# Kernel tuning notes

Measured on AMD Instinct MI355X. Metric: run time of the kernel, lower is better.

Reference implementation:

```python
import jax, jax.numpy as jnp
import numpy as np

L, D, DC, T, FF = 512, 512, 256, 128, 2048
P_COEF = 0.5


def layernorm(x, g, b):
    m = jnp.mean(x, axis=-1, keepdims=True)
    v = jnp.mean((x - m) ** 2, axis=-1, keepdims=True)
    return (x - m) / jnp.sqrt(v + 1e-5) * g + b


def conv_pool(t, w):
    # t: (L, N, D); torch attention_pool: permute -> (N, L, D), Conv1d over channels=L, length=D
    x = jnp.transpose(t, (1, 0, 2))  # (N, L, D)
    y = jax.lax.conv_general_dilated(x, w, window_strides=(2,), padding=[(1, 1)],
                                     dimension_numbers=("NCH", "OIH", "NCH"))
    return jnp.transpose(y, (1, 0, 2))  # (L, N, D//2)


def attn_fused(q, k):
    # q: (L, 1, d), k: (M, 1, d); faithful to module.attention with N=1 (squeeze(1))
    q2, k2 = q[:, 0], k[:, 0]
    scale = 1.0 / jnp.sqrt(jnp.asarray(q2.shape[1], q2.dtype))
    a = jax.nn.softmax((q2 @ k2.T) * scale, axis=-1)
    return (a @ k2 + q2)[:, None, :]  # fused residual add of q


def setup_inputs() -> dict:
    key = jax.random.key(0)
    ks = jax.random.split(key, 8)
    x = jax.random.normal(ks[0], (L, 1, D), jnp.float32)
    cached_k = jax.random.normal(ks[1], (T, L, 1, DC), jnp.float32)
    mem_mask = jax.random.randint(ks[2], (T,), 0, 2, jnp.int32)
    return {
        "x": x,
        "cached_k": cached_k,
        "ln1_g": jnp.ones((D,), jnp.float32),
        "ln1_b": jnp.zeros((D,), jnp.float32),
        "ln2_g": jnp.ones((D,), jnp.float32),
        "ln2_b": jnp.zeros((D,), jnp.float32),
        "w_compress_k": jax.random.normal(ks[3], (L, L, 3), jnp.float32) * (1.0 / np.sqrt(3 * L)),
        "w_compress_cur": jax.random.normal(ks[4], (L, L, 3), jnp.float32) * (1.0 / np.sqrt(3 * L)),
        "ap_w": jax.random.normal(ks[5], (DC, D), jnp.float32) * (1.0 / np.sqrt(DC)),
        "ap_b": jnp.zeros((D,), jnp.float32),
        "fc_w": jax.random.normal(ks[6], (D, FF), jnp.float32) * (1.0 / np.sqrt(D)),
        "fc_b": jnp.zeros((FF,), jnp.float32),
        "proj_w": jax.random.normal(ks[7], (FF, D), jnp.float32) * (1.0 / np.sqrt(FF)),
        "proj_b": jnp.zeros((D,), jnp.float32),
        "mem_mask": mem_mask,
    }


def reference(x, cached_k, ln1_g, ln1_b, ln2_g, ln2_b, w_compress_k, w_compress_cur,
              ap_w, ap_b, fc_w, fc_b, proj_w, proj_b, mem_mask):
    x1 = layernorm(x, ln1_g, ln1_b)                      # ln_1; q = k = x1
    # mask_memory: zero cached entries whose video name differs (per-entry, N=1)
    mem = cached_k * mem_mask.astype(x.dtype)[:, None, None, None]  # (T, L, 1, DC)
    k_cur = conv_pool(x1, w_compress_cur)                # (L, 1, DC) compress current k
    k = jnp.concatenate([mem.reshape(-1, 1, DC), k_cur], axis=0)    # ((T+1)*L, 1, DC)
    q = conv_pool(x1, w_compress_k)                      # k.shape[2]==256 branch: compress q
    selfatten = attn_fused(q, q)
    atten = attn_fused(q, k) + selfatten * P_COEF
    atten = atten @ ap_w + ap_b                          # attenproj 256 -> 512
    x2 = x1 + atten
    h = layernorm(x2, ln2_g, ln2_b)
    h = h @ fc_w + fc_b
    h = h * jax.nn.sigmoid(1.702 * h)                    # QuickGELU
    h = h @ proj_w + proj_b
    return x2 + h
```

## Files before the change

### kernel.cpp

```cpp
#include <hip/hip_runtime.h>
#include <hip/hip_bf16.h>

typedef unsigned short u16;
typedef unsigned int u32;
typedef __attribute__((ext_vector_type(8))) short bf16x8;
typedef __attribute__((ext_vector_type(4))) short bf16x4;
typedef __attribute__((ext_vector_type(4))) float f32x4;
typedef __attribute__((ext_vector_type(8))) u16 u16x8;
typedef __attribute__((ext_vector_type(4))) u16 u16x4;
typedef __attribute__((ext_vector_type(4))) u32 u32x4;

__device__ __forceinline__ u16 f2bf(float x){
  __hip_bfloat16 h = __float2bfloat16(x);
  return __builtin_bit_cast(u16, h);
}
__device__ __forceinline__ float bf2f(u16 u){
  __hip_bfloat16 h = __builtin_bit_cast(__hip_bfloat16, u);
  return __bfloat162float(h);
}

template<bool BF>
__global__ __launch_bounds__(256) void ln_kernel(const float* __restrict__ in,
    const float* __restrict__ g, const float* __restrict__ b,
    float* __restrict__ outf, u16* __restrict__ outb)
{
  int row = blockIdx.x, tid = threadIdx.x;
  const float* p = in + (size_t)row*512 + tid*2;
  float v0 = p[0], v1 = p[1];
  float s = v0+v1, ss = v0*v0+v1*v1;
  #pragma unroll
  for (int o=1;o<64;o<<=1){ s += __shfl_xor(s,o); ss += __shfl_xor(ss,o); }
  __shared__ float rs[4], rss[4];
  if ((tid&63)==0){ rs[tid>>6]=s; rss[tid>>6]=ss; }
  __syncthreads();
  s = rs[0]+rs[1]+rs[2]+rs[3]; ss = rss[0]+rss[1]+rss[2]+rss[3];
  float mean = s*(1.f/512.f);
  float var  = ss*(1.f/512.f) - mean*mean;
  float rstd = 1.f/sqrtf(var + 1e-5f);
  int d = tid*2;
  float o0 = (v0-mean)*rstd*g[d]   + b[d];
  float o1 = (v1-mean)*rstd*g[d+1] + b[d+1];
  if (BF){
    outb[(size_t)row*512+d]   = f2bf(o0);
    outb[(size_t)row*512+d+1] = f2bf(o1);
  } else {
    outf[(size_t)row*512+d]   = o0;
    outf[(size_t)row*512+d+1] = o1;
  }
}

__global__ __launch_bounds__(256) void xgT_kernel(const float* __restrict__ x1, u16* __restrict__ xgT)
{
  int h = blockIdx.x, tid = threadIdx.x;
  #pragma unroll
  for (int rep=0;rep<6;rep++){
    int k = rep*256 + tid;
    int i = k/3, kk = k - i*3;
    int pos = 2*h - 1 + kk;
    float v = (pos >= 0 && pos < 512) ? x1[(size_t)i*512 + pos] : 0.f;
    xgT[(size_t)h*1536 + k] = f2bf(v);
  }
}

__device__ __forceinline__ void transcvt_body(float (*t)[33],
    const float* __restrict__ in, u16* __restrict__ out, int K, int N, int bx, int by)
{
  int nb = bx*32, kb = by*32;
  int tx = threadIdx.x & 31, ty = threadIdx.x >> 5;
  #pragma unroll
  for (int i=0;i<32;i+=8) t[ty+i][tx] = in[(size_t)(kb+ty+i)*N + nb+tx];
  __syncthreads();
  #pragma unroll
  for (int i=0;i<32;i+=8) out[(size_t)(nb+ty+i)*K + kb+tx] = f2bf(t[tx][ty+i]);
}

__global__ __launch_bounds__(256) void prep_kernel(
    const float* __restrict__ x, const float* __restrict__ ln1g, const float* __restrict__ ln1b,
    const float* __restrict__ wk, const float* __restrict__ wc,
    const float* __restrict__ apw, const float* __restrict__ fcw, const float* __restrict__ pjw,
    const float* __restrict__ ck, const int* __restrict__ mask,
    float* __restrict__ x1,
    u16* __restrict__ wkcb, u16* __restrict__ apT, u16* __restrict__ fcT,
    u16* __restrict__ pjT, u16* __restrict__ kbf)
{
  __shared__ float t[32][33];
  __shared__ float rs[4], rss[4];
  int b = blockIdx.x, tid = threadIdx.x;
  if (b < 512){
    const float* p = x + (size_t)b*512 + tid*2;
    float v0 = p[0], v1 = p[1];
    float s = v0+v1, ss = v0*v0+v1*v1;
    #pragma unroll
    for (int o=1;o<64;o<<=1){ s += __shfl_xor(s,o); ss += __shfl_xor(ss,o); }
    if ((tid&63)==0){ rs[tid>>6]=s; rss[tid>>6]=ss; }
    __syncthreads();
    s = rs[0]+rs[1]+rs[2]+rs[3]; ss = rss[0]+rss[1]+rss[2]+rss[3];
    float mean = s*(1.f/512.f);
    float var  = ss*(1.f/512.f) - mean*mean;
    float rstd = 1.f/sqrtf(var + 1e-5f);
    int d = tid*2;
    x1[(size_t)b*512+d]   = (v0-mean)*rstd*ln1g[d]   + ln1b[d];
    x1[(size_t)b*512+d+1] = (v1-mean)*rstd*ln1g[d+1] + ln1b[d+1];
  } else if (b < 8704){
    int flat = (b-512)*256 + tid;
    int row = flat >> 5, seg = flat & 31;
    if (mask[row>>9] == 0) return;
    const float* src = ck + (size_t)row*256 + seg*8;
    u16x8 o;
    #pragma unroll
    for (int j=0;j<8;j++) o[j] = f2bf(src[j]);
    *(u16x8*)(kbf + (size_t)row*256 + seg*8) = o;
  } else if (b < 9472){
    size_t i = (size_t)((b-8704)*256 + tid)*8;
    const size_t half = (size_t)512*1536;
    const float* src = (i < half) ? (wk + i) : (wc + (i - half));
    u16x8 o;
    #pragma unroll
    for (int j=0;j<8;j++) o[j] = f2bf(src[j]);
    *(u16x8*)(wkcb + i) = o;
  } else if (b < 9600){
    int f = b - 9472;
    transcvt_body(t, apw, apT, 256, 512, f & 15, f >> 4);
  } else if (b < 10624){
    int f = b - 9600;
    transcvt_body(t, fcw, fcT, 512, 2048, f & 63, f >> 6);
  } else {
    int f = b - 10624;
    transcvt_body(t, pjw, pjT, 2048, 512, f & 15, f >> 4);
  }
}

template<int ACT, bool WF32, bool WBF, int W>
__global__ __launch_bounds__(64*W) void gemm4(
    const u16* __restrict__ A, const u16* __restrict__ B,
    const float* __restrict__ bias, const float* __restrict__ resid,
    float* __restrict__ outF, u16* __restrict__ outB, u16* __restrict__ outB2,
    int rowSplit, int M, int N, int K)
{
  __shared__ float red[W][32][33];
  int tid = threadIdx.x;
  int w = tid >> 6, lane = tid & 63;
  int lq = lane & 15, lg = lane >> 4;
  int m0 = blockIdx.y*32, n0 = blockIdx.x*32;
  int Ks = K / W;
  int kbeg = w * Ks;
  f32x4 acc00={0,0,0,0}, acc01={0,0,0,0}, acc10={0,0,0,0}, acc11={0,0,0,0};
  const u16* pa0 = A + (size_t)(m0+lq)*K + kbeg + lg*8;
  const u16* pa1 = pa0 + (size_t)16*K;
  const u16* pb0 = B + (size_t)(n0+lq)*K + kbeg + lg*8;
  const u16* pb1 = pb0 + (size_t)16*K;
  #pragma unroll 2
  for (int k0=0;k0<Ks;k0+=32){
    bf16x8 a0 = *(const bf16x8*)(pa0+k0);
    bf16x8 a1 = *(const bf16x8*)(pa1+k0);
    bf16x8 b0 = *(const bf16x8*)(pb0+k0);
    bf16x8 b1 = *(const bf16x8*)(pb1+k0);
    acc00 = __builtin_amdgcn_mfma_f32_16x16x32_bf16(a0,b0,acc00,0,0,0);
    acc01 = __builtin_amdgcn_mfma_f32_16x16x32_bf16(a0,b1,acc01,0,0,0);
    acc10 = __builtin_amdgcn_mfma_f32_16x16x32_bf16(a1,b0,acc10,0,0,0);
    acc11 = __builtin_amdgcn_mfma_f32_16x16x32_bf16(a1,b1,acc11,0,0,0);
  }
  f32x4 accs[2][2] = {{acc00,acc01},{acc10,acc11}};
  #pragma unroll
  for (int mi=0;mi<2;mi++)
    #pragma unroll
    for (int ni=0;ni<2;ni++)
      #pragma unroll
      for (int r=0;r<4;r++)
        red[w][mi*16+lg*4+r][ni*16+lq] = accs[mi][ni][r];
  __syncthreads();
  #pragma unroll
  for (int rr=0;rr<16/W;rr++){
    int cell = rr*64*W + tid;
    int row = cell >> 5, col = cell & 31;
    float v = 0.f;
    #pragma unroll
    for (int ww=0;ww<W;ww++) v += red[ww][row][col];
    int grow = m0 + row, gcol = n0 + col;
    if (bias)  v += bias[gcol];
    if (ACT==1) v = v/(1.f+__expf(-1.702f*v));
    if (resid) v += resid[(size_t)grow*N+gcol];
    if (WF32) outF[(size_t)grow*N+gcol] = v;
    if (WBF){
      if (grow < rowSplit) outB[(size_t)grow*N+gcol] = f2bf(v);
      else                 outB2[(size_t)(grow-rowSplit)*N+gcol] = f2bf(v);
    }
  }
}

__global__ __launch_bounds__(128) void attn_flash(
    const u16* __restrict__ qb, const u16* __restrict__ keys,
    const int* __restrict__ mask,
    u16* __restrict__ pO, float* __restrict__ pL)
{
  __shared__ u16 kv[2][8192];
  int tid = threadIdx.x;
  int w = tid >> 6, lane = tid & 63, lq = lane & 15, lg = lane >> 4;
  int c = blockIdx.x, qt = blockIdx.y;
  const u16* kp = keys;
  int kstart = c * 1024, off = 0, nt = 32;
  if (c == 65) { kp = qb; kstart = 0; nt = 16; }
  else if (c == 64) { kstart = 65536; nt = 16; }
  else {
    int m0 = mask[2*c], m1 = mask[2*c+1];
    if (!m0 && !m1) return;
    off = m0 ? 0 : 512;
    nt = ((m0 && m1) ? 32 : 16);
  }
  int qbase = qt*32 + w*16;

  bf16x8 qf[8];
  {
    const u16* qrow = qb + (size_t)(qbase+lq)*256 + lg*8;
    #pragma unroll
    for (int s=0;s<8;s++) qf[s] = *(const bf16x8*)(qrow + s*32);
  }
  f32x4 o[16];
  #pragma unroll
  for (int i=0;i<16;i++) o[i] = (f32x4){0,0,0,0};
  float l_acc = 0.f;

  auto kv3 = (__attribute__((address_space(3))) char*)&kv[0][0];
  unsigned kvaddr0 = (unsigned)(unsigned long long)kv3;
  const char* gbase = (const char*)kp + (size_t)(kstart+off)*512;

  #define STAGE(i, b) { \
    const char* tb = gbase + (size_t)(i)*16384; \
    _Pragma("unroll") \
    for (int rep=0; rep<8; rep++){ \
      int slot = rep*128 + tid; \
      int goff = ((slot&63)>>1)*512 + ((slot>>6)*16 + (slot&1)*8)*2; \
      __builtin_amdgcn_global_load_lds( \
        (const __attribute__((address_space(1))) unsigned*)(tb + goff), \
        (__attribute__((address_space(3))) unsigned*)(kv3 + (b)*16384 + (rep*128 + (tid & ~63))*16), \
        16, 0, 0); \
    } }

  #define ISSUE8(T, ab) \
    asm volatile( \
      "ds_read_b64_tr_b16 %0, %8 offset:0\n\t" \
      "ds_read_b64_tr_b16 %1, %8 offset:512\n\t" \
      "ds_read_b64_tr_b16 %2, %8 offset:1024\n\t" \
      "ds_read_b64_tr_b16 %3, %8 offset:1536\n\t" \
      "ds_read_b64_tr_b16 %4, %8 offset:2048\n\t" \
      "ds_read_b64_tr_b16 %5, %8 offset:2560\n\t" \
      "ds_read_b64_tr_b16 %6, %8 offset:3072\n\t" \
      "ds_read_b64_tr_b16 %7, %8 offset:3584\n\t" \
      : "=&v"(T[0]),"=&v"(T[1]),"=&v"(T[2]),"=&v"(T[3]), \
        "=&v"(T[4]),"=&v"(T[5]),"=&v"(T[6]),"=&v"(T[7]) \
      : "v"(ab) : "memory")

  #define MFMA4(T, base) { \
    bf16x8 v0_ = __builtin_shufflevector(T[0],T[1],0,1,2,3,4,5,6,7); \
    bf16x8 v1_ = __builtin_shufflevector(T[2],T[3],0,1,2,3,4,5,6,7); \
    bf16x8 v2_ = __builtin_shufflevector(T[4],T[5],0,1,2,3,4,5,6,7); \
    bf16x8 v3_ = __builtin_shufflevector(T[6],T[7],0,1,2,3,4,5,6,7); \
    o[(base)+0] = __builtin_amdgcn_mfma_f32_16x16x32_bf16(pa, v0_, o[(base)+0], 0,0,0); \
    o[(base)+1] = __builtin_amdgcn_mfma_f32_16x16x32_bf16(pa, v1_, o[(base)+1], 0,0,0); \
    o[(base)+2] = __builtin_amdgcn_mfma_f32_16x16x32_bf16(pa, v2_, o[(base)+2], 0,0,0); \
    o[(base)+3] = __builtin_amdgcn_mfma_f32_16x16x32_bf16(pa, v3_, o[(base)+3], 0,0,0); \
  }

  STAGE(0, 0);
  for (int i=0; i<nt; i++){
    int cur = i & 1;
    if (i+1 < nt){
      STAGE(i+1, cur^1);
      asm volatile("s_waitcnt vmcnt(8)" ::: "memory");
    } else {
      asm volatile("s_waitcnt vmcnt(0)" ::: "memory");
    }
    __syncthreads();

    const u16* kb = &kv[cur][0];
    f32x4 s0 = {0,0,0,0}, s1 = {0,0,0,0};
    #pragma unroll
    for (int s=0;s<8;s++){
      int e = (2*s + (lg>>1))*512 + lq*16 + (lg&1)*8;
      bf16x8 ka0 = *(const bf16x8*)(kb + e);
      bf16x8 ka1 = *(const bf16x8*)(kb + e + 256);
      s0 = __builtin_amdgcn_mfma_f32_16x16x32_bf16(ka0, qf[s], s0, 0,0,0);
      s1 = __builtin_amdgcn_mfma_f32_16x16x32_bf16(ka1, qf[s], s1, 0,0,0);
    }
    asm volatile("s_waitcnt lgkmcnt(0)" ::: "memory");

    unsigned trb = kvaddr0 + cur*16384 + lane*8;
    bf16x4 tA[8], tB[8], tC[8], tD[8];
    ISSUE8(tA, trb);
    ISSUE8(tB, trb + 4096);

    float p[8];
    #pragma unroll
    for (int r=0;r<4;r++){ p[r]   = __expf(s0[r]*0.0625f);
                           p[4+r] = __expf(s1[r]*0.0625f); }
    l_acc += (p[0]+p[1])+(p[2]+p[3])+((p[4]+p[5])+(p[6]+p[7]));
    u32 w0 = (u32)f2bf(p[0]) | ((u32)f2bf(p[1])<<16);
    u32 w1 = (u32)f2bf(p[2]) | ((u32)f2bf(p[3])<<16);
    u32 w2 = (u32)f2bf(p[4]) | ((u32)f2bf(p[5])<<16);
    u32 w3 = (u32)f2bf(p[6]) | ((u32)f2bf(p[7])<<16);
    u32x4 fq = {w0,w1,w2,w3};
    bf16x8 pa = __builtin_bit_cast(bf16x8, fq);

    asm volatile("s_waitcnt lgkmcnt(8)" ::: "memory");
    __builtin_amdgcn_sched_barrier(0);
    MFMA4(tA, 0);
    ISSUE8(tC, trb + 8192);
    asm volatile("s_waitcnt lgkmcnt(8)" ::: "memory");
    __builtin_amdgcn_sched_barrier(0);
    MFMA4(tB, 4);
    ISSUE8(tD, trb + 12288);
    asm volatile("s_waitcnt lgkmcnt(8)" ::: "memory");
    __builtin_amdgcn_sched_barrier(0);
    MFMA4(tC, 8);
    asm volatile("s_waitcnt lgkmcnt(0)" ::: "memory");
    __builtin_amdgcn_sched_barrier(0);
    MFMA4(tD, 12);
    __syncthreads();
  }
  #undef STAGE
  #undef ISSUE8
  #undef MFMA4

  l_acc += __shfl_xor(l_acc, 16);
  l_acc += __shfl_xor(l_acc, 32);
  size_t qrow = (size_t)c*512 + qbase;
  if (lane < 16) pL[qrow + lq] = l_acc;
  #pragma unroll
  for (int dt=0; dt<16; dt++){
    #pragma unroll
    for (int r=0;r<4;r++){
      pO[(qrow + lg*4 + r)*256 + dt*16 + lq] = f2bf(o[dt][r]);
    }
  }
}

__global__ __launch_bounds__(256) void attn_reduce(
    const u16* __restrict__ pO, const float* __restrict__ pL,
    const int* __restrict__ mask, const u16* __restrict__ qb,
    u16* __restrict__ attn_out)
{
  __shared__ f32x4 redO[4][64];
  __shared__ float redL[4];
  __shared__ float scnt[2];
  int q = blockIdx.x, tid = threadIdx.x;
  int cg = tid >> 6, dq = tid & 63;

  float mz = (tid < 128) ? ((mask[tid]==0) ? 1.f : 0.f) : 0.f;
  #pragma unroll
  for (int o=1;o<64;o<<=1) mz += __shfl_xor(mz, o);
  if ((tid&63)==0 && tid < 128) scnt[tid>>6] = mz;

  f32x4 acc = {0,0,0,0};
  float lsum = 0.f;
  for (int c = cg; c < 65; c += 4){
    bool valid = (c==64) || mask[2*c] || mask[2*c+1];
    if (!valid) continue;
    u16x4 v = *(const u16x4*)(pO + ((size_t)c*512+q)*256 + dq*4);
    acc[0] += bf2f(v[0]); acc[1] += bf2f(v[1]);
    acc[2] += bf2f(v[2]); acc[3] += bf2f(v[3]);
    if (dq==0) lsum += pL[(size_t)c*512+q];
  }
  redO[cg][dq] = acc;
  if (dq==0) redL[cg] = lsum;
  __syncthreads();
  if (tid < 64){
    f32x4 s = redO[0][tid];
    f32x4 s1 = redO[1][tid], s2 = redO[2][tid], s3 = redO[3][tid];
    s[0]+=s1[0]+s2[0]+s3[0]; s[1]+=s1[1]+s2[1]+s3[1];
    s[2]+=s1[2]+s2[2]+s3[2]; s[3]+=s1[3]+s2[3]+s3[3];
    float den = redL[0]+redL[1]+redL[2]+redL[3] + 512.f*(scnt[0]+scnt[1]);
    float ls  = pL[(size_t)65*512 + q];
    u16x4 sv = *(const u16x4*)(pO + ((size_t)65*512+q)*256 + tid*4);
    u16x4 qv = *(const u16x4*)(qb + (size_t)q*256 + tid*4);
    u16x4 ov;
    #pragma unroll
    for (int j=0;j<4;j++)
      ov[j] = f2bf(s[j]/den + 0.5f*bf2f(sv[j])/ls + 1.5f*bf2f(qv[j]));
    *(u16x4*)(attn_out + (size_t)q*256 + tid*4) = ov;
  }
}

extern "C" void kernel_launch(void* const* d_in, const int* in_sizes, int n_in,
                              void* d_out, int out_size, void* d_ws, size_t ws_size,
                              hipStream_t stream)
{
  const float* x    = (const float*)d_in[0];
  const float* ck   = (const float*)d_in[1];
  const float* ln1g = (const float*)d_in[2];
  const float* ln1b = (const float*)d_in[3];
  const float* ln2g = (const float*)d_in[4];
  const float* ln2b = (const float*)d_in[5];
  const float* wk   = (const float*)d_in[6];
  const float* wc   = (const float*)d_in[7];
  const float* apw  = (const float*)d_in[8];
  const float* apb  = (const float*)d_in[9];
  const float* fcw  = (const float*)d_in[10];
  const float* fcb  = (const float*)d_in[11];
  const float* pjw  = (const float*)d_in[12];
  const float* pjb  = (const float*)d_in[13];
  const int*   mask = (const int*)d_in[14];
  float* out = (float*)d_out;

  char* wsb = (char*)d_ws;
  float* x1    = (float*)(wsb + 0);
  float* x2    = (float*)(wsb + 1048576);
  u16*   aoutb = (u16*)  (wsb + 2097152);
  u16*   x2nb  = (u16*)  (wsb + 2359296);
  u16*   xgT   = (u16*)  (wsb + 2883584);
  u16*   apT   = (u16*)  (wsb + 3670016);
  u16*   fcT   = (u16*)  (wsb + 3932160);
  u16*   pjT   = (u16*)  (wsb + 6029312);
  u16*   qbf   = (u16*)  (wsb + 8126464);
  u16*   kbf   = (u16*)  (wsb + 8388608);
  float* pL    = (float*)(wsb + 42205184);
  u16*   pO    = (u16*)  (wsb + 42340352);
  u16*   wkcb  = (u16*)  (wsb + 42340352);
  u16*   hb    = (u16*)  (wsb + 42340352);

  prep_kernel<<<11648,256,0,stream>>>(x, ln1g, ln1b, wk, wc, apw, fcw, pjw, ck, mask,
      x1, wkcb, apT, fcT, pjT, kbf);
  xgT_kernel<<<256,256,0,stream>>>(x1, xgT);

  gemm4<0,false,true,8><<<dim3(8,32),512,0,stream>>>(wkcb, xgT, nullptr, nullptr,
      nullptr, qbf, kbf + (size_t)65536*256, 512, 1024, 256, 1536);

  attn_flash<<<dim3(66,16),128,0,stream>>>(qbf, kbf, mask, pO, pL);
  attn_reduce<<<512,256,0,stream>>>(pO, pL, mask, qbf, aoutb);

  gemm4<0,true,false,4><<<dim3(16,16),256,0,stream>>>(aoutb, apT, apb, x1,
      x2, nullptr, nullptr, 512, 512, 512, 256);
  ln_kernel<true><<<512,256,0,stream>>>(x2, ln2g, ln2b, nullptr, x2nb);
  gemm4<1,false,true,4><<<dim3(64,16),256,0,stream>>>(x2nb, fcT, fcb, nullptr,
      nullptr, hb, hb, 4096, 512, 2048, 512);
  gemm4<0,true,false,8><<<dim3(16,16),512,0,stream>>>(hb, pjT, pjb, x2,
      out, nullptr, nullptr, 512, 512, 512, 2048);
}
```

Before: 113.9 us.

## Move weight transpose-convert blocks from prep kernel into attention kernel grid

The transpose-and-bf16-convert work for the attenproj, fc and proj weights moves out of the prep kernel and into extra blocks appended to the attention kernel's flattened 1D grid. Those blocks reuse the attention shared memory as the transpose tile and run with 128 threads, so each covers its 32x32 tile in eight passes instead of four. The aim is to shorten the serial prep stage and let this weight work fill idle CUs while attention runs, since many attention blocks exit early on masked chunks. The cost is more work inside the attention launch, which could delay attention blocks that do real work.

```diff
diff --git a/kernel.cpp b/kernel.cpp
--- a/kernel.cpp
+++ b/kernel.cpp
@@ -62,28 +62,24 @@
   }
 }
 
-__device__ __forceinline__ void transcvt_body(float (*t)[33],
+__device__ __forceinline__ void transcvt128(float (*t)[33],
     const float* __restrict__ in, u16* __restrict__ out, int K, int N, int bx, int by)
 {
   int nb = bx*32, kb = by*32;
   int tx = threadIdx.x & 31, ty = threadIdx.x >> 5;
   #pragma unroll
-  for (int i=0;i<32;i+=8) t[ty+i][tx] = in[(size_t)(kb+ty+i)*N + nb+tx];
+  for (int i=0;i<32;i+=4) t[ty+i][tx] = in[(size_t)(kb+ty+i)*N + nb+tx];
   __syncthreads();
   #pragma unroll
-  for (int i=0;i<32;i+=8) out[(size_t)(nb+ty+i)*K + kb+tx] = f2bf(t[tx][ty+i]);
+  for (int i=0;i<32;i+=4) out[(size_t)(nb+ty+i)*K + kb+tx] = f2bf(t[tx][ty+i]);
 }
 
 __global__ __launch_bounds__(256) void prep_kernel(
     const float* __restrict__ x, const float* __restrict__ ln1g, const float* __restrict__ ln1b,
     const float* __restrict__ wk, const float* __restrict__ wc,
-    const float* __restrict__ apw, const float* __restrict__ fcw, const float* __restrict__ pjw,
     const float* __restrict__ ck, const int* __restrict__ mask,
-    float* __restrict__ x1,
-    u16* __restrict__ wkcb, u16* __restrict__ apT, u16* __restrict__ fcT,
-    u16* __restrict__ pjT, u16* __restrict__ kbf)
-{
-  __shared__ float t[32][33];
+    float* __restrict__ x1, u16* __restrict__ wkcb, u16* __restrict__ kbf)
+{
   __shared__ float rs[4], rss[4];
   int b = blockIdx.x, tid = threadIdx.x;
   if (b < 512){
@@ -110,7 +106,7 @@
     #pragma unroll
     for (int j=0;j<8;j++) o[j] = f2bf(src[j]);
     *(u16x8*)(kbf + (size_t)row*256 + seg*8) = o;
-  } else if (b < 9472){
+  } else {
     size_t i = (size_t)((b-8704)*256 + tid)*8;
     const size_t half = (size_t)512*1536;
     const float* src = (i < half) ? (wk + i) : (wc + (i - half));
@@ -118,15 +114,6 @@
     #pragma unroll
     for (int j=0;j<8;j++) o[j] = f2bf(src[j]);
     *(u16x8*)(wkcb + i) = o;
-  } else if (b < 9600){
-    int f = b - 9472;
-    transcvt_body(t, apw, apT, 256, 512, f & 15, f >> 4);
-  } else if (b < 10624){
-    int f = b - 9600;
-    transcvt_body(t, fcw, fcT, 512, 2048, f & 63, f >> 6);
-  } else {
-    int f = b - 10624;
-    transcvt_body(t, pjw, pjT, 2048, 512, f & 15, f >> 4);
   }
 }
 
@@ -191,12 +178,23 @@
 __global__ __launch_bounds__(128) void attn_flash(
     const u16* __restrict__ qb, const u16* __restrict__ keys,
     const int* __restrict__ mask,
+    const float* __restrict__ apw, const float* __restrict__ fcw, const float* __restrict__ pjw,
+    u16* __restrict__ apT, u16* __restrict__ fcT, u16* __restrict__ pjT,
     u16* __restrict__ pO, float* __restrict__ pL)
 {
   __shared__ u16 kv[2][8192];
   int tid = threadIdx.x;
+  int bid = blockIdx.x;
+  if (bid >= 1056){
+    int f = bid - 1056;
+    float (*t)[33] = reinterpret_cast<float(*)[33]>(&kv[0][0]);
+    if (f < 128)       transcvt128(t, apw, apT, 256, 512, f & 15, f >> 4);
+    else if (f < 1152) transcvt128(t, fcw, fcT, 512, 2048, (f-128) & 63, (f-128) >> 6);
+    else               transcvt128(t, pjw, pjT, 2048, 512, (f-1152) & 15, (f-1152) >> 4);
+    return;
+  }
   int w = tid >> 6, lane = tid & 63, lq = lane & 15, lg = lane >> 4;
-  int c = blockIdx.x, qt = blockIdx.y;
+  int c = bid % 66, qt = bid / 66;
   const u16* kp = keys;
   int kstart = c * 1024, off = 0, nt = 32;
   if (c == 65) { kp = qb; kstart = 0; nt = 16; }
@@ -417,14 +415,13 @@
   u16*   wkcb  = (u16*)  (wsb + 42340352);
   u16*   hb    = (u16*)  (wsb + 42340352);
 
-  prep_kernel<<<11648,256,0,stream>>>(x, ln1g, ln1b, wk, wc, apw, fcw, pjw, ck, mask,
-      x1, wkcb, apT, fcT, pjT, kbf);
+  prep_kernel<<<9472,256,0,stream>>>(x, ln1g, ln1b, wk, wc, ck, mask, x1, wkcb, kbf);
   xgT_kernel<<<256,256,0,stream>>>(x1, xgT);
 
   gemm4<0,false,true,8><<<dim3(8,32),512,0,stream>>>(wkcb, xgT, nullptr, nullptr,
       nullptr, qbf, kbf + (size_t)65536*256, 512, 1024, 256, 1536);
 
-  attn_flash<<<dim3(66,16),128,0,stream>>>(qbf, kbf, mask, pO, pL);
+  attn_flash<<<3232,128,0,stream>>>(qbf, kbf, mask, apw, fcw, pjw, apT, fcT, pjT, pO, pL);
   attn_reduce<<<512,256,0,stream>>>(pO, pL, mask, qbf, aoutb);
 
   gemm4<0,true,false,4><<<dim3(16,16),256,0,stream>>>(aoutb, apT, apb, x1,
```

New measurement: 112.9 us. No clear change (-0.9%).
